# Kernel optimization log

Measured on AMD Instinct MI355X. Metric: run time of the kernel, lower is better.

The kernel has to match this reference:

```python
import jax, jax.numpy as jnp
import numpy as np

B, C, N, L = 64, 32, 500, 12
C_OUT = 32
C_CAT = 9 * C  # (order*(support_len+1)+1)*c_in = 288


def setup_inputs() -> dict:
    key = jax.random.key(0)
    ks = jax.random.split(key, 7)
    x = jax.random.normal(ks[0], (B, C, N, L), dtype=jnp.float32)
    # row-stochastic-ish adjacencies: scale by 1/N to keep hops numerically tame
    A0 = jax.random.uniform(ks[1], (N, N), dtype=jnp.float32) / N
    A1 = jax.random.uniform(ks[2], (N, N), dtype=jnp.float32) / N
    A2 = jax.random.uniform(ks[3], (N, N), dtype=jnp.float32) / N
    A3 = jax.random.uniform(ks[4], (B, N, N), dtype=jnp.float32) / N
    W = jax.random.normal(ks[5], (C_OUT, C_CAT), dtype=jnp.float32) * 0.05
    b = jax.random.normal(ks[6], (C_OUT,), dtype=jnp.float32) * 0.05
    return {"x": x, "A0": A0, "A1": A1, "A2": A2, "A3": A3, "W": W, "b": b}


def reference(x, A0, A1, A2, A3, W, b):
    # x: [B, C, N, L]; A0..A2: [N, N]; A3: [B, N, N]; W: [C_OUT, 9*C]; b: [C_OUT]
    def hop2(h, A):  # static adjacency
        return jnp.einsum('ncvl,vw->ncwl', h, A)

    def hop3(h, A):  # batched (dynamic) adjacency
        return jnp.einsum('ncvl,nvw->ncwl', h, A)

    out = [x]
    for A in (A0, A1, A2):
        x1 = hop2(x, A)
        x2 = hop2(x1, A)
        out.extend([x1, x2])
    x1 = hop3(x, A3)
    x2 = hop3(x1, A3)
    out.extend([x1, x2])

    h = jnp.concatenate(out, axis=1)  # [B, 9C, N, L]
    # 1x1 Conv2d == channel mixing matmul + bias
    h = jnp.einsum('ncvl,oc->novl', h, W) + b[None, :, None, None]
    # dropout in eval mode: identity
    return h
```

## Files before the change

kernel.cpp:

```cpp
#include <hip/hip_runtime.h>

typedef unsigned short u16;
typedef __bf16 bf16x8 __attribute__((ext_vector_type(8)));
typedef float f32x4 __attribute__((ext_vector_type(4)));
typedef const unsigned int __attribute__((address_space(1))) gu32;
typedef unsigned int __attribute__((address_space(3))) lu32;

#define NN 500
#define LLc 12
#define CC 32
#define MM 384
#define KP 512
#define MT 96
#define NT2 128
#define XS_S 40
#define AS_S 40
#define CT2_S 136
#define TS_S 384
#define AT_ELS 256000
#define HM_G 12288000L
#define HM_B 192000L
#define HCL_G 12582912L
#define HCL_B 196608L

__device__ __forceinline__ u16 f2bf(float f) {
    union { float f; unsigned u; } cv; cv.f = f;
    unsigned u = cv.u;
    u += 0x7fffu + ((u >> 16) & 1u);
    return (u16)(u >> 16);
}
__device__ __forceinline__ float bf2f(u16 s) {
    union { unsigned u; float f; } cv; cv.u = ((unsigned)s) << 16;
    return cv.f;
}

__global__ __launch_bounds__(256) void prep_all(
    const float* __restrict__ x,
    const float* __restrict__ A0, const float* __restrict__ A1,
    const float* __restrict__ A2, const float* __restrict__ A3,
    u16* __restrict__ At_s, u16* __restrict__ At_b,
    u16* __restrict__ Xt, u16* __restrict__ Xm,
    const float* __restrict__ W, u16* __restrict__ Wp)
{
    __shared__ u16 Ls[MM * 36];
    const int id = blockIdx.x;
    const int t = threadIdx.x;

    if (id < 17152) {
        int rem = id & 255;
        int z  = id >> 8;
        int n0 = (rem & 15) * 32;
        int k0 = (rem >> 4) * 32;
        const float* Ab; u16* Ob;
        if (z == 0)      { Ab = A0; Ob = At_s; }
        else if (z == 1) { Ab = A1; Ob = At_s + (long)AT_ELS; }
        else if (z == 2) { Ab = A2; Ob = At_s + 2L * AT_ELS; }
        else             { Ab = A3 + (long)(z - 3) * NN * NN; Ob = At_b + (long)(z - 3) * AT_ELS; }
        {
            int vl = t >> 3, u = t & 7;
            float4 v = make_float4(0.f, 0.f, 0.f, 0.f);
            if (k0 + vl < NN && n0 + 4 * u + 4 <= NN)
                v = *(const float4*)(Ab + (long)(k0 + vl) * NN + n0 + 4 * u);
            int nb = 4 * u;
            Ls[(nb + 0) * 36 + vl] = f2bf(v.x);
            Ls[(nb + 1) * 36 + vl] = f2bf(v.y);
            Ls[(nb + 2) * 36 + vl] = f2bf(v.z);
            Ls[(nb + 3) * 36 + vl] = f2bf(v.w);
        }
        __syncthreads();
        {
            int row = t >> 3, u = t & 7;
            if (n0 + row < NN)
                *(uint2*)(Ob + (long)(n0 + row) * KP + k0 + 4 * u) = *(const uint2*)(&Ls[row * 36 + 4 * u]);
        }
    } else if (id < 18176) {
        int jj = id - 17152;
        int v0 = (jj & 15) * 32;
        int b  = jj >> 4;
        #pragma unroll
        for (int j = 0; j < 12; ++j) {
            int f = t + 256 * j;
            int c = f / 96;
            int r = f - c * 96;
            int vl = r / 3;
            int l3 = (r - vl * 3) * 4;
            float4 v = make_float4(0.f, 0.f, 0.f, 0.f);
            if (v0 + vl < NN)
                v = *(const float4*)(x + ((long)b * CC + c) * (NN * LLc) + (long)(v0 + vl) * LLc + l3);
            int mb = (c * LLc + l3) * 36 + vl;
            Ls[mb]       = f2bf(v.x);
            Ls[mb + 36]  = f2bf(v.y);
            Ls[mb + 72]  = f2bf(v.z);
            Ls[mb + 108] = f2bf(v.w);
        }
        __syncthreads();
        #pragma unroll
        for (int j = 0; j < 12; ++j) {
            int f = t + 256 * j;
            int row = f >> 3, u = f & 7;
            *(uint2*)(Xt + ((long)b * MM + row) * KP + v0 + 4 * u) = *(const uint2*)(&Ls[row * 36 + 4 * u]);
        }
        if (Xm) {
            u16* Xb = Xm + (long)b * HM_B;
            #pragma unroll
            for (int j = 0; j < 6; ++j) {
                int f = t + 256 * j;
                int vl = f & 31;
                int lq = f >> 5;
                int l  = lq % 12;
                int cq = lq / 12;
                if (v0 + vl < NN) {
                    union { u16 s[8]; uint4 v; } pk;
                    #pragma unroll
                    for (int c8 = 0; c8 < 8; ++c8)
                        pk.s[c8] = Ls[((cq * 8 + c8) * 12 + l) * 36 + vl];
                    *(uint4*)(Xb + ((long)(l * NN + v0 + vl)) * 32 + cq * 8) = pk.v;
                }
            }
        }
    } else {
        int idx = (id - 18176) * 256 + t;
        int j    = idx & 7;
        int lane = (idx >> 3) & 63;
        int p    = (idx >> 9) & 1;
        int mt   = (idx >> 10) & 1;
        int g    = idx >> 11;
        int o  = mt * 16 + (lane & 15);
        int kk = g * 32 + (lane >> 4) * 8 + j;
        float wv = W[o * 288 + kk];
        u16 hi = f2bf(wv);
        Wp[idx] = (p == 0) ? hi : f2bf(wv - bf2f(hi));
    }
}

__global__ __launch_bounds__(256, 3) void hop_fast8(
    const u16* __restrict__ Xsrc, long x_gstride, long x_bstride,
    const u16* __restrict__ At_s,
    const u16* __restrict__ At_b,
    u16* __restrict__ Hcl,
    u16* __restrict__ HmArg)
{
    __shared__ __align__(16) u16 smem[21504];
    u16* Ct = smem;

    const int t = threadIdx.x;
    const int lane = t & 63;
    const int wv = t >> 6;
    const int f0 = blockIdx.x + 4 * (blockIdx.y + 4 * blockIdx.z);
    const int w  = (f0 & 7) * 2048 + (f0 >> 3);
    const int zc = w >> 4;
    const int rem = w & 15;
    const int bx = rem & 3;
    const int my = rem >> 2;
    const int g  = zc & 3;
    const int b  = zc >> 2;
    const int n0 = bx * NT2;
    const int m0 = my * 96;
    const int cb = my * 8;
    const int ln  = lane & 15;
    const int q16 = lane >> 4;

    const u16* Ab = (g < 3) ? (At_s + (long)g * AT_ELS) : (At_b + (long)b * AT_ELS);
    const u16* Xb = Xsrc + (long)g * x_gstride + (long)b * x_bstride;

    const int rbase = lane >> 2;
    const int coff  = (((lane & 3) ^ ((lane >> 3) & 3)) << 3);
    const int rsel  = ((q16 ^ ((ln >> 1) & 3)) << 3);

    auto STAGE = [&](int kk, int pb) {
        char* base = (char*)smem + pb * 14336;
        if (wv < 2) {
            #pragma unroll
            for (int j = 0; j < 4; ++j) {
                int r16 = wv * 4 + j;
                const u16* src = Ab + (long)(n0 + r16 * 16 + rbase) * KP + kk + coff;
                __builtin_amdgcn_global_load_lds((gu32*)src, (lu32*)(base + r16 * 1024), 16, 0, 0);
            }
        } else {
            #pragma unroll
            for (int j = 0; j < 3; ++j) {
                int r16 = (wv - 2) * 3 + j;
                const u16* src = Xb + (long)(m0 + r16 * 16 + rbase) * KP + kk + coff;
                __builtin_amdgcn_global_load_lds((gu32*)src, (lu32*)(base + 8192 + r16 * 1024), 16, 0, 0);
            }
        }
    };

    f32x4 acc[2][6];
    #pragma unroll
    for (int ns = 0; ns < 2; ++ns)
        #pragma unroll
        for (int i = 0; i < 6; ++i)
            #pragma unroll
            for (int r = 0; r < 4; ++r) acc[ns][i][r] = 0.f;

    auto COMPUTE = [&](int pb) {
        const u16* As = smem + pb * 7168;
        const u16* Xs = As + 4096;
        bf16x8 b0 = *(const bf16x8*)(&As[(wv * 32 + ln) * 32 + rsel]);
        bf16x8 b1 = *(const bf16x8*)(&As[(wv * 32 + 16 + ln) * 32 + rsel]);
        __builtin_amdgcn_s_setprio(1);
        #pragma unroll
        for (int i = 0; i < 6; ++i) {
            bf16x8 af = *(const bf16x8*)(&Xs[(i * 16 + ln) * 32 + rsel]);
            acc[0][i] = __builtin_amdgcn_mfma_f32_16x16x32_bf16(af, b0, acc[0][i], 0, 0, 0);
            acc[1][i] = __builtin_amdgcn_mfma_f32_16x16x32_bf16(af, b1, acc[1][i], 0, 0, 0);
        }
        __builtin_amdgcn_s_setprio(0);
    };

    STAGE(0, 0);
    STAGE(32, 1);
    int c0 = 0, c1 = 1, c2 = 2;
    #pragma unroll 1
    for (int s = 0; s < 15; ++s) {
        if (wv < 2) asm volatile("s_waitcnt vmcnt(4)" ::: "memory");
        else        asm volatile("s_waitcnt vmcnt(3)" ::: "memory");
        __builtin_amdgcn_s_barrier();
        __builtin_amdgcn_sched_barrier(0);
        if (s <= 13) STAGE(32 * (s + 2), c2);
        COMPUTE(c0);
        int tmp = c0; c0 = c1; c1 = c2; c2 = tmp;
    }
    asm volatile("s_waitcnt vmcnt(0)" ::: "memory");
    __builtin_amdgcn_s_barrier();
    __builtin_amdgcn_sched_barrier(0);
    COMPUTE(c0);

    __syncthreads();
    #pragma unroll
    for (int ns = 0; ns < 2; ++ns) {
        int col = wv * 32 + ns * 16 + ln;
        #pragma unroll
        for (int i6 = 0; i6 < 6; ++i6) {
            int rb = i6 * 16 + (lane >> 4) * 4;
            #pragma unroll
            for (int r = 0; r < 4; ++r)
                Ct[(rb + r) * CT2_S + col] = f2bf(acc[ns][i6][r]);
        }
    }
    __syncthreads();
    if (Hcl) {
        u16* Ocl = Hcl + (long)g * HCL_G + (long)b * HCL_B;
        #pragma unroll
        for (int j = 0; j < 12; ++j) {
            int f = t + 256 * j;
            int row = f >> 5, u = f & 31;
            int n = n0 + 4 * u;
            uint2 v = make_uint2(0u, 0u);
            if (n < NN) v = *(const uint2*)(&Ct[row * CT2_S + 4 * u]);
            *(uint2*)(Ocl + (long)(m0 + row) * KP + n) = v;
        }
    }
    {
        u16* Om = HmArg + (long)g * HM_G + (long)b * HM_B;
        #pragma unroll
        for (int j = 0; j < 6; ++j) {
            int f = t + 256 * j;
            int n_l = f & 127;
            int l   = f >> 7;
            int n = n0 + n_l;
            if (n < NN) {
                union { u16 s[8]; uint4 v; } pk;
                #pragma unroll
                for (int c8 = 0; c8 < 8; ++c8)
                    pk.s[c8] = Ct[(c8 * 12 + l) * CT2_S + n_l];
                *(uint4*)(Om + ((long)(l * NN + n)) * 32 + cb) = pk.v;
            }
        }
    }
}

__global__ __launch_bounds__(256, 3) void hop_fast7(
    const u16* __restrict__ Xsrc, long x_gstride, long x_bstride,
    const u16* __restrict__ At_s,
    const u16* __restrict__ At_b,
    u16* __restrict__ Hout, long h_gstride)
{
    __shared__ __align__(16) u16 smem[24576];
    u16* Ct = smem;

    const int t = threadIdx.x;
    const int lane = t & 63;
    const int wv = t >> 6;
    const int f0 = blockIdx.x + 4 * (blockIdx.y + 3 * blockIdx.z);
    const int w  = (f0 & 7) * 384 + (f0 >> 3);
    const int zc = w / 12;
    const int rem = w - zc * 12;
    const int bx = rem & 3;
    const int by = rem >> 2;
    const int g  = zc & 3;
    const int b  = zc >> 2;
    const int n0 = bx * 128;
    const int m0 = by * 128;
    const int ln  = lane & 15;
    const int q16 = lane >> 4;

    const u16* Ab = (g < 3) ? (At_s + (long)g * AT_ELS) : (At_b + (long)b * AT_ELS);
    const u16* Xb = Xsrc + (long)g * x_gstride + (long)b * x_bstride;
    u16* Ob = Hout + (long)g * h_gstride + (long)b * ((long)MM * KP);

    const int rbase = lane >> 2;
    const int coff  = (((lane & 3) ^ ((lane >> 3) & 3)) << 3);
    const int rsel  = ((q16 ^ ((ln >> 1) & 3)) << 3);

    auto STAGE = [&](int kk, int pb) {
        #pragma unroll
        for (int j = 0; j < 4; ++j) {
            int o = (wv * 4 + j) << 10;
            const u16* src;
            if (o < 8192) src = Ab + (long)(n0 + (o >> 6) + rbase) * KP + kk + coff;
            else          src = Xb + (long)(m0 + (o >> 6) - 128 + rbase) * KP + kk + coff;
            __builtin_amdgcn_global_load_lds((gu32*)src,
                (lu32*)((char*)smem + pb * 16384 + o), 16, 0, 0);
        }
    };

    f32x4 acc[2][8];
    #pragma unroll
    for (int ns = 0; ns < 2; ++ns)
        #pragma unroll
        for (int i = 0; i < 8; ++i)
            #pragma unroll
            for (int r = 0; r < 4; ++r) acc[ns][i][r] = 0.f;

    auto COMPUTE = [&](int pb) {
        const u16* As = smem + pb * 8192;
        const u16* Xs = As + 4096;
        bf16x8 b0 = *(const bf16x8*)(&As[(wv * 32 + ln) * 32 + rsel]);
        bf16x8 b1 = *(const bf16x8*)(&As[(wv * 32 + 16 + ln) * 32 + rsel]);
        __builtin_amdgcn_s_setprio(1);
        #pragma unroll
        for (int i = 0; i < 8; ++i) {
            bf16x8 af = *(const bf16x8*)(&Xs[(i * 16 + ln) * 32 + rsel]);
            acc[0][i] = __builtin_amdgcn_mfma_f32_16x16x32_bf16(af, b0, acc[0][i], 0, 0, 0);
            acc[1][i] = __builtin_amdgcn_mfma_f32_16x16x32_bf16(af, b1, acc[1][i], 0, 0, 0);
        }
        __builtin_amdgcn_s_setprio(0);
    };

    STAGE(0, 0);
    STAGE(32, 1);
    int c0 = 0, c1 = 1, c2 = 2;
    #pragma unroll 1
    for (int s = 0; s < 15; ++s) {
        asm volatile("s_waitcnt vmcnt(4)" ::: "memory");
        __builtin_amdgcn_s_barrier();
        __builtin_amdgcn_sched_barrier(0);
        if (s <= 13) STAGE(32 * (s + 2), c2);
        COMPUTE(c0);
        int tmp = c0; c0 = c1; c1 = c2; c2 = tmp;
    }
    asm volatile("s_waitcnt vmcnt(0)" ::: "memory");
    __builtin_amdgcn_s_barrier();
    __builtin_amdgcn_sched_barrier(0);
    COMPUTE(c0);

    #pragma unroll
    for (int h = 0; h < 2; ++h) {
        __syncthreads();
        #pragma unroll
        for (int ns = 0; ns < 2; ++ns) {
            int col = wv * 32 + ns * 16 + ln;
            #pragma unroll
            for (int i4 = 0; i4 < 4; ++i4) {
                int rb = i4 * 16 + (lane >> 4) * 4;
                #pragma unroll
                for (int r = 0; r < 4; ++r)
                    Ct[(rb + r) * CT2_S + col] = f2bf(acc[ns][h * 4 + i4][r]);
            }
        }
        __syncthreads();
        #pragma unroll
        for (int j = 0; j < 8; ++j) {
            int f = t + 256 * j;
            int row = f >> 5, u = f & 31;
            int n = n0 + 4 * u;
            uint2 v = make_uint2(0u, 0u);
            if (n < NN) v = *(const uint2*)(&Ct[row * CT2_S + 4 * u]);
            *(uint2*)(Ob + (long)(m0 + h * 64 + row) * KP + n) = v;
        }
    }
}

__global__ __launch_bounds__(512, 4) void mix_stream(
    const u16* __restrict__ Xm,
    const u16* __restrict__ Hm,
    const u16* __restrict__ Wp,
    const float* __restrict__ bias,
    float* __restrict__ out)
{
    __shared__ __align__(16) float Ct[12496];

    const int t   = threadIdx.x;
    const int wg  = blockIdx.y * 8 + blockIdx.x;
    const int swz = (wg & 7) * 64 + (wg >> 3);
    const int bx  = swz & 7;
    const int b   = swz >> 3;
    const int n0  = bx * 64;
    const int w    = t >> 6;
    const int lane = t & 63;
    const int kq   = lane >> 4;
    const int ln   = lane & 15;

    f32x4 acc[6][2];
    #pragma unroll
    for (int i = 0; i < 6; ++i)
        #pragma unroll
        for (int m = 0; m < 2; ++m)
            #pragma unroll
            for (int r = 0; r < 4; ++r) acc[i][m][r] = 0.f;

    #pragma unroll 1
    for (int g = 0; g < 9; ++g) {
        const u16* src;
        if (g == 0) src = Xm + (long)b * HM_B;
        else {
            int gg = g - 1;
            int buf = (gg & 1) ? 4 + (gg >> 1) : (gg >> 1);
            src = Hm + (long)buf * HM_G + (long)b * HM_B;
        }
        uint4 wf[2][2];
        #pragma unroll
        for (int mt = 0; mt < 2; ++mt)
            #pragma unroll
            for (int p = 0; p < 2; ++p)
                wf[mt][p] = *(const uint4*)(Wp + ((((g * 2 + mt) * 2 + p) * 64 + lane) * 8));
        #pragma unroll
        for (int i = 0; i < 6; ++i) {
            int ct = w * 6 + i;
            int l  = ct >> 2;
            int n  = n0 + ((ct & 3) << 4) + ln;
            uint4 fbv = make_uint4(0u, 0u, 0u, 0u);
            if (n < NN) fbv = *(const uint4*)(src + ((long)(l * NN + n)) * 32 + kq * 8);
            bf16x8 fb = *(const bf16x8*)&fbv;
            acc[i][0] = __builtin_amdgcn_mfma_f32_16x16x32_bf16(*(const bf16x8*)&wf[0][0], fb, acc[i][0], 0, 0, 0);
            acc[i][0] = __builtin_amdgcn_mfma_f32_16x16x32_bf16(*(const bf16x8*)&wf[0][1], fb, acc[i][0], 0, 0, 0);
            acc[i][1] = __builtin_amdgcn_mfma_f32_16x16x32_bf16(*(const bf16x8*)&wf[1][0], fb, acc[i][1], 0, 0, 0);
            acc[i][1] = __builtin_amdgcn_mfma_f32_16x16x32_bf16(*(const bf16x8*)&wf[1][1], fb, acc[i][1], 0, 0, 0);
        }
    }

    #pragma unroll
    for (int mt = 0; mt < 2; ++mt) {
        __syncthreads();
        #pragma unroll
        for (int i = 0; i < 6; ++i) {
            int col = (w * 6 + i) * 16 + ln;
            #pragma unroll
            for (int r = 0; r < 4; ++r)
                Ct[(kq * 4 + r) * 781 + col] = acc[i][mt][r];
        }
        __syncthreads();
        int o16 = t >> 5, u = t & 31;
        int og = mt * 16 + o16;
        float bs = bias[og];
        float* ob = out + (((long)b * CC + og) * NN + n0) * 12L;
        #pragma unroll
        for (int j2 = 0; j2 < 2; ++j2) {
            int n = u + 32 * j2;
            if (n0 + n < NN) {
                float v[12];
                #pragma unroll
                for (int l = 0; l < 12; ++l) v[l] = Ct[o16 * 781 + l * 64 + n] + bs;
                #pragma unroll
                for (int q = 0; q < 3; ++q)
                    *(float4*)(ob + (long)n * 12 + q * 4) = *(const float4*)&v[q * 4];
            }
        }
    }
}

__global__ __launch_bounds__(512, 4) void mix_mfma(
    const u16* __restrict__ Xt,
    const u16* __restrict__ H,
    const u16* __restrict__ Wp,
    const float* __restrict__ bias,
    float* __restrict__ out,
    long h_gs, long h_bs, int h_rs)
{
    __shared__ __align__(16) char smem[50176];
    u16*   Ls = (u16*)smem;
    float* Ct = (float*)smem;

    const int t   = threadIdx.x;
    const int wg  = blockIdx.y * 8 + blockIdx.x;
    const int swz = (wg & 7) * 64 + (wg >> 3);
    const int bx  = swz & 7;
    const int b   = swz >> 3;
    const int n0  = bx * 64;
    const int w    = t >> 6;
    const int lane = t & 63;
    const int kq   = lane >> 4;
    const int ln   = lane & 15;
    const int srow   = lane >> 3;
    const int schunk = (lane & 7) * 8;

    f32x4 acc[6][2];
    #pragma unroll
    for (int i = 0; i < 6; ++i)
        #pragma unroll
        for (int m = 0; m < 2; ++m)
            #pragma unroll
            for (int r = 0; r < 4; ++r) acc[i][m][r] = 0.f;

    #pragma unroll 1
    for (int g = 0; g < 9; ++g) {
        const u16* base; int rs;
        if (g == 0) { base = Xt + (long)b * (MM * KP); rs = KP; }
        else {
            int gg = g - 1;
            int buf = (gg & 1) ? 4 + (gg >> 1) : (gg >> 1);
            base = H + (long)buf * h_gs + (long)b * h_bs; rs = h_rs;
        }
        __syncthreads();
        #pragma unroll
        for (int i = 0; i < 6; ++i) {
            int r0 = (w * 6 + i) * 8;
            const u16* src = base + (long)(r0 + srow) * rs + n0 + schunk;
            __builtin_amdgcn_global_load_lds((gu32*)src, (lu32*)(Ls + r0 * 64), 16, 0, 0);
        }
        asm volatile("s_waitcnt vmcnt(0)" ::: "memory");
        __syncthreads();
        uint4 wf[2][2];
        #pragma unroll
        for (int mt = 0; mt < 2; ++mt)
            #pragma unroll
            for (int p = 0; p < 2; ++p)
                wf[mt][p] = *(const uint4*)(Wp + ((((g * 2 + mt) * 2 + p) * 64 + lane) * 8));
        #pragma unroll
        for (int i = 0; i < 6; ++i) {
            int ct = w * 6 + i;
            int off0 = kq * 6144 + (ct >> 2) * 64 + (ct & 3) * 16 + ln;
            union { u16 s[8]; bf16x8 v; } fb;
            #pragma unroll
            for (int j = 0; j < 8; ++j) fb.s[j] = Ls[off0 + j * 768];
            #pragma unroll
            for (int mt = 0; mt < 2; ++mt) {
                acc[i][mt] = __builtin_amdgcn_mfma_f32_16x16x32_bf16(*(const bf16x8*)&wf[mt][0], fb.v, acc[i][mt], 0, 0, 0);
                acc[i][mt] = __builtin_amdgcn_mfma_f32_16x16x32_bf16(*(const bf16x8*)&wf[mt][1], fb.v, acc[i][mt], 0, 0, 0);
            }
        }
    }

    #pragma unroll
    for (int mt = 0; mt < 2; ++mt) {
        __syncthreads();
        #pragma unroll
        for (int i = 0; i < 6; ++i) {
            int col = (w * 6 + i) * 16 + ln;
            #pragma unroll
            for (int r = 0; r < 4; ++r)
                Ct[(kq * 4 + r) * 781 + col] = acc[i][mt][r];
        }
        __syncthreads();
        int o16 = t >> 5, u = t & 31;
        int og = mt * 16 + o16;
        float bs = bias[og];
        float* ob = out + (((long)b * CC + og) * NN + n0) * 12L;
        #pragma unroll
        for (int j2 = 0; j2 < 2; ++j2) {
            int n = u + 32 * j2;
            if (n0 + n < NN) {
                float v[12];
                #pragma unroll
                for (int l = 0; l < 12; ++l) v[l] = Ct[o16 * 781 + l * 64 + n] + bs;
                #pragma unroll
                for (int q = 0; q < 3; ++q)
                    *(float4*)(ob + (long)n * 12 + q * 4) = *(const float4*)&v[q * 4];
            }
        }
    }
}

__global__ __launch_bounds__(256) void atrans_all(
    const float* __restrict__ A0, const float* __restrict__ A1,
    const float* __restrict__ A2, const float* __restrict__ A3,
    u16* __restrict__ At_s, u16* __restrict__ At_b)
{
    __shared__ u16 Ls[32 * 36];
    const int t = threadIdx.x;
    const int n0 = blockIdx.x * 32;
    const int k0 = blockIdx.y * 32;
    const int z = blockIdx.z;
    const float* Ab; u16* Ob;
    if (z == 0)      { Ab = A0; Ob = At_s; }
    else if (z == 1) { Ab = A1; Ob = At_s + (long)AT_ELS; }
    else if (z == 2) { Ab = A2; Ob = At_s + 2L * AT_ELS; }
    else             { Ab = A3 + (long)(z - 3) * NN * NN; Ob = At_b + (long)(z - 3) * AT_ELS; }
    {
        int vl = t >> 3, u = t & 7;
        float4 v = make_float4(0.f, 0.f, 0.f, 0.f);
        if (k0 + vl < NN && n0 + 4 * u + 4 <= NN)
            v = *(const float4*)(Ab + (long)(k0 + vl) * NN + n0 + 4 * u);
        int nb = 4 * u;
        Ls[(nb + 0) * 36 + vl] = f2bf(v.x);
        Ls[(nb + 1) * 36 + vl] = f2bf(v.y);
        Ls[(nb + 2) * 36 + vl] = f2bf(v.z);
        Ls[(nb + 3) * 36 + vl] = f2bf(v.w);
    }
    __syncthreads();
    {
        int row = t >> 3, u = t & 7;
        if (n0 + row < NN)
            *(uint2*)(Ob + (long)(n0 + row) * KP + k0 + 4 * u) = *(const uint2*)(&Ls[row * 36 + 4 * u]);
    }
}

__global__ __launch_bounds__(256) void xpose_kernel(
    const float* __restrict__ x, u16* __restrict__ Xt)
{
    __shared__ u16 Ls[MM * 36];
    const int t = threadIdx.x;
    const int v0 = blockIdx.x * 32;
    const int b  = blockIdx.y;
    #pragma unroll
    for (int j = 0; j < 12; ++j) {
        int f = t + 256 * j;
        int c = f / 96;
        int r = f - c * 96;
        int vl = r / 3;
        int l3 = (r - vl * 3) * 4;
        float4 v = make_float4(0.f, 0.f, 0.f, 0.f);
        if (v0 + vl < NN)
            v = *(const float4*)(x + ((long)b * CC + c) * (NN * LLc) + (long)(v0 + vl) * LLc + l3);
        int mb = (c * LLc + l3) * 36 + vl;
        Ls[mb]       = f2bf(v.x);
        Ls[mb + 36]  = f2bf(v.y);
        Ls[mb + 72]  = f2bf(v.z);
        Ls[mb + 108] = f2bf(v.w);
    }
    __syncthreads();
    #pragma unroll
    for (int j = 0; j < 12; ++j) {
        int f = t + 256 * j;
        int row = f >> 3, u = f & 7;
        *(uint2*)(Xt + ((long)b * MM + row) * KP + v0 + 4 * u) = *(const uint2*)(&Ls[row * 36 + 4 * u]);
    }
}

__global__ __launch_bounds__(256, 4) void hop_fast(
    const u16* __restrict__ Xsrc, long x_bstride, int x_rstride, int x_klim,
    const u16* __restrict__ At,   long a_bstride,
    u16* __restrict__ hout)
{
    __shared__ __align__(16) u16 smem[13056];
    u16* As = smem;
    u16* Xs = smem + 5120;
    u16* Ct = smem;

    const int t = threadIdx.x;
    const int lane = t & 63;
    const int wv = t >> 6;
    const int n0 = blockIdx.x * NT2;
    const int m0 = blockIdx.y * MT;
    const int b  = blockIdx.z;
    const int ln = lane & 15;
    const int q8 = (lane >> 4) * 8;

    const u16* Ab = At + (long)b * a_bstride;
    const u16* Xb = Xsrc + (long)b * x_bstride;

    uint2 pa[4], px[3];
    auto loadA = [&](int k0) {
        #pragma unroll
        for (int j = 0; j < 4; ++j) {
            int f = t + 256 * j;
            int n = f >> 3, u = f & 7;
            uint2 v = make_uint2(0u, 0u);
            if (n0 + n < NN)
                v = *(const uint2*)(Ab + (long)(n0 + n) * KP + k0 + 4 * u);
            pa[j] = v;
        }
    };
    auto loadX = [&](int k0) {
        #pragma unroll
        for (int j = 0; j < 3; ++j) {
            int f = t + 256 * j;
            int r = f >> 3, u = f & 7;
            int k = k0 + 4 * u;
            uint2 v = make_uint2(0u, 0u);
            if (k < x_klim)
                v = *(const uint2*)(Xb + (long)(m0 + r) * x_rstride + k);
            px[j] = v;
        }
    };

    f32x4 acc[2][6];
    #pragma unroll
    for (int ns = 0; ns < 2; ++ns)
        #pragma unroll
        for (int i = 0; i < 6; ++i)
            #pragma unroll
            for (int r = 0; r < 4; ++r) acc[ns][i][r] = 0.f;

    loadA(0);
    loadX(0);
    #pragma unroll 1
    for (int s = 0; s < 16; ++s) {
        __syncthreads();
        #pragma unroll
        for (int j = 0; j < 4; ++j) {
            int f = t + 256 * j;
            *(uint2*)(&As[(f >> 3) * AS_S + 4 * (f & 7)]) = pa[j];
        }
        #pragma unroll
        for (int j = 0; j < 3; ++j) {
            int f = t + 256 * j;
            *(uint2*)(&Xs[(f >> 3) * XS_S + 4 * (f & 7)]) = px[j];
        }
        if (s < 15) {
            loadA(32 * (s + 1));
            loadX(32 * (s + 1));
        }
        __syncthreads();
        bf16x8 af[6];
        #pragma unroll
        for (int i = 0; i < 6; ++i)
            af[i] = *(const bf16x8*)(&Xs[(i * 16 + ln) * XS_S + q8]);
        #pragma unroll
        for (int ns = 0; ns < 2; ++ns) {
            bf16x8 bfr = *(const bf16x8*)(&As[(wv * 32 + ns * 16 + ln) * AS_S + q8]);
            #pragma unroll
            for (int i = 0; i < 6; ++i)
                acc[ns][i] = __builtin_amdgcn_mfma_f32_16x16x32_bf16(af[i], bfr, acc[ns][i], 0, 0, 0);
        }
    }

    __syncthreads();
    #pragma unroll
    for (int ns = 0; ns < 2; ++ns) {
        int col = wv * 32 + ns * 16 + ln;
        #pragma unroll
        for (int i = 0; i < 6; ++i) {
            int rb = i * 16 + (lane >> 4) * 4;
            #pragma unroll
            for (int r = 0; r < 4; ++r)
                Ct[(rb + r) * CT2_S + col] = f2bf(acc[ns][i][r]);
        }
    }
    __syncthreads();
    u16* Ob = hout + (long)b * ((long)MM * NN);
    #pragma unroll
    for (int j = 0; j < 12; ++j) {
        int f = t + 256 * j;
        int row = f >> 5, u = f & 31;
        int n = n0 + 4 * u;
        if (n < NN)
            *(uint2*)(Ob + (long)(m0 + row) * NN + n) = *(const uint2*)(&Ct[row * CT2_S + 4 * u]);
    }
}

__global__ __launch_bounds__(256, 2) void mix_kernel(
    const float* __restrict__ x,
    const u16* __restrict__ h1,
    const u16* __restrict__ h2,
    const float* __restrict__ W,
    const float* __restrict__ bias,
    int blk1, int blk2,
    float* __restrict__ out, int init)
{
    __shared__ __align__(16) float smem[CC * TS_S + 3 * 1056];
    float* ts = smem;
    float* Ws = smem + CC * TS_S;

    const int t = threadIdx.x;
    const int b = blockIdx.y;
    const int w0 = blockIdx.x * 32;
    const int o  = t & 15;
    const int wg = (t >> 4) & 7;
    const int lh = t >> 7;

    #pragma unroll
    for (int j = 0; j < 4; ++j) {
        int f = t + 256 * j;
        int oo = f & 31, c = f >> 5;
        Ws[c * 33 + oo]        = W[oo * 288 + blk1 * 32 + c];
        Ws[1056 + c * 33 + oo] = W[oo * 288 + blk2 * 32 + c];
        if (init) Ws[2112 + c * 33 + oo] = W[oo * 288 + c];
    }

    float acc2[2][4][6];
    #pragma unroll
    for (int a = 0; a < 2; ++a)
        #pragma unroll
        for (int q = 0; q < 4; ++q)
            #pragma unroll
            for (int l = 0; l < 6; ++l) acc2[a][q][l] = 0.f;

    auto stage_h = [&](const u16* h) {
        #pragma unroll
        for (int j = 0; j < 12; ++j) {
            int f = t + 256 * j;
            int row = f >> 3, u = f & 7;
            int w = w0 + 4 * u;
            uint2 raw = make_uint2(0u, 0u);
            if (w < NN)
                raw = *(const uint2*)(h + ((long)b * MM + row) * NN + w);
            int c = row / 12;
            int l = row - c * 12;
            float* dst = &ts[c * TS_S + l * 32 + 4 * u];
            dst[0] = bf2f((u16)(raw.x & 0xffffu));
            dst[1] = bf2f((u16)(raw.x >> 16));
            dst[2] = bf2f((u16)(raw.y & 0xffffu));
            dst[3] = bf2f((u16)(raw.y >> 16));
        }
    };
    auto accum = [&](const float* Wg) {
        for (int c = 0; c < CC; ++c) {
            float w1 = Wg[c * 33 + o];
            float w2 = Wg[c * 33 + o + 16];
            #pragma unroll
            for (int l6 = 0; l6 < 6; ++l6) {
                const float4 hv = *(const float4*)(&ts[c * TS_S + (lh * 6 + l6) * 32 + wg * 4]);
                acc2[0][0][l6] += w1 * hv.x;
                acc2[0][1][l6] += w1 * hv.y;
                acc2[0][2][l6] += w1 * hv.z;
                acc2[0][3][l6] += w1 * hv.w;
                acc2[1][0][l6] += w2 * hv.x;
                acc2[1][1][l6] += w2 * hv.y;
                acc2[1][2][l6] += w2 * hv.z;
                acc2[1][3][l6] += w2 * hv.w;
            }
        }
    };

    if (init) {
        #pragma unroll
        for (int j = 0; j < 12; ++j) {
            int f = t + 256 * j;
            int c = f / 96;
            int r = f - c * 96;
            int w = r / 3;
            int q = r - w * 3;
            float4 v = make_float4(0.f, 0.f, 0.f, 0.f);
            if (w0 + w < NN)
                v = *(const float4*)(x + ((long)b * CC + c) * (NN * LLc) + (long)(w0 + w) * LLc + q * 4);
            float* dst = &ts[c * TS_S + (q * 4) * 32 + w];
            dst[0]  = v.x; dst[32] = v.y; dst[64] = v.z; dst[96] = v.w;
        }
        __syncthreads();
        accum(Ws + 2112);
        __syncthreads();
    }
    stage_h(h1);
    __syncthreads();
    accum(Ws);
    __syncthreads();
    stage_h(h2);
    __syncthreads();
    accum(Ws + 1056);

    #pragma unroll
    for (int oh = 0; oh < 2; ++oh) {
        int oo = o + 16 * oh;
        float bs = init ? bias[oo] : 0.f;
        #pragma unroll
        for (int q = 0; q < 4; ++q) {
            int w = w0 + wg * 4 + q;
            if (w < NN) {
                float* op = out + ((long)b * CC + oo) * (NN * LLc) + (long)w * LLc + lh * 6;
                #pragma unroll
                for (int p = 0; p < 3; ++p) {
                    float2* pp = (float2*)op + p;
                    float2 v;
                    if (init) {
                        v.x = bs + acc2[oh][q][2 * p];
                        v.y = bs + acc2[oh][q][2 * p + 1];
                    } else {
                        v = *pp;
                        v.x += acc2[oh][q][2 * p];
                        v.y += acc2[oh][q][2 * p + 1];
                    }
                    *pp = v;
                }
            }
        }
    }
}

extern "C" void kernel_launch(void* const* d_in, const int* in_sizes, int n_in,
                              void* d_out, int out_size, void* d_ws, size_t ws_size,
                              hipStream_t stream) {
    const float* x    = (const float*)d_in[0];
    const float* A0   = (const float*)d_in[1];
    const float* A1   = (const float*)d_in[2];
    const float* A2   = (const float*)d_in[3];
    const float* A3   = (const float*)d_in[4];
    const float* W    = (const float*)d_in[5];
    const float* bias = (const float*)d_in[6];
    float* out = (float*)d_out;
    char* ws = (char*)d_ws;

    const size_t AT_BYTES  = (size_t)AT_ELS * 2;
    const size_t A3T_BYTES = 64 * AT_BYTES;
    const size_t XT_BYTES  = (size_t)64 * MM * KP * 2;
    const size_t WPK_BYTES = 36864;
    const size_t HB2_ELS   = (size_t)64 * MM * KP;
    const size_t H8B_PAD   = 8 * HB2_ELS * 2;
    const size_t need4 = H8B_PAD + 3 * AT_BYTES + A3T_BYTES + XT_BYTES + WPK_BYTES;

    const size_t HCL_BYTES = 4 * HB2_ELS * 2;
    const size_t HM_BYTES  = 8 * (size_t)HM_G * 2;
    const size_t XM_BYTES  = 64 * (size_t)HM_B * 2;
    const size_t need5 = HCL_BYTES + HM_BYTES + 3 * AT_BYTES + A3T_BYTES
                       + XT_BYTES + XM_BYTES + WPK_BYTES;

    dim3 blk(256);

    if (ws_size >= need5) {
        u16* Hcl  = (u16*)ws;
        u16* Hm   = (u16*)(ws + HCL_BYTES);
        u16* At_s = (u16*)(ws + HCL_BYTES + HM_BYTES);
        u16* A3t  = At_s + 3L * AT_ELS;
        u16* Xt   = (u16*)((char*)A3t + A3T_BYTES);
        u16* Xm   = Xt + (size_t)64 * MM * KP;
        u16* Wpk  = Xm + 64 * (size_t)HM_B;

        prep_all<<<dim3(18248), blk, 0, stream>>>(x, A0, A1, A2, A3, At_s, A3t, Xt, Xm, W, Wpk);
        hop_fast8<<<dim3(4, 4, 1024), blk, 0, stream>>>(
            Xt, 0L, (long)MM * KP, At_s, A3t, Hcl, Hm);
        hop_fast8<<<dim3(4, 4, 1024), blk, 0, stream>>>(
            Hcl, (long)HCL_G, (long)HCL_B, At_s, A3t, (u16*)nullptr, Hm + 4 * HM_G);
        mix_stream<<<dim3(8, 64), dim3(512), 0, stream>>>(Xm, Hm, Wpk, bias, out);
        return;
    }

    if (ws_size >= need4) {
        u16* Hb   = (u16*)ws;
        u16* At_s = (u16*)(ws + H8B_PAD);
        u16* A3t  = At_s + 3L * AT_ELS;
        u16* Xt   = (u16*)(ws + H8B_PAD + 3 * AT_BYTES + A3T_BYTES);
        u16* Wpk  = Xt + (size_t)64 * MM * KP;

        prep_all<<<dim3(18248), blk, 0, stream>>>(x, A0, A1, A2, A3, At_s, A3t, Xt, (u16*)nullptr, W, Wpk);
        hop_fast7<<<dim3(4, 3, 256), blk, 0, stream>>>(
            Xt, 0L, (long)MM * KP, At_s, A3t, Hb, (long)HB2_ELS);
        hop_fast7<<<dim3(4, 3, 256), blk, 0, stream>>>(
            Hb, (long)HB2_ELS, (long)MM * KP, At_s, A3t,
            Hb + 4 * HB2_ELS, (long)HB2_ELS);
        mix_mfma<<<dim3(8, 64), dim3(512), 0, stream>>>(
            Xt, Hb, Wpk, bias, out, (long)HB2_ELS, (long)MM * KP, KP);
        return;
    }

    const size_t HBUF_ELS  = (size_t)64 * MM * NN;
    const size_t H_BYTES   = HBUF_ELS * 2;
    const size_t need_at   = 2 * H_BYTES + 3 * AT_BYTES + A3T_BYTES;

    u16* H1 = (u16*)ws;
    u16* H2 = (u16*)(ws + H_BYTES);
    u16* At0 = (u16*)(ws + 2 * H_BYTES);
    u16* A3t = At0 + 3L * AT_ELS;
    u16* Xt  = (u16*)(ws + need_at);

    dim3 fgrid(4, 4, 64);
    dim3 mgrid(16, 64);

    xpose_kernel<<<dim3(16, 64), blk, 0, stream>>>(x, Xt);
    atrans_all<<<dim3(16, 16, 67), blk, 0, stream>>>(A0, A1, A2, A3, At0, A3t);

    const long XT_BS = (long)MM * KP;
    const long H_BS  = (long)MM * NN;
    u16* Atp[4] = {At0, At0 + (long)AT_ELS, At0 + 2L * AT_ELS, A3t};

    for (int i = 0; i < 4; ++i) {
        long a_bs = (i == 3) ? (long)AT_ELS : 0;
        hop_fast<<<fgrid, blk, 0, stream>>>(Xt, XT_BS, KP, KP, Atp[i], a_bs, H1);
        hop_fast<<<fgrid, blk, 0, stream>>>(H1, H_BS, NN, NN, Atp[i], a_bs, H2);
        mix_kernel<<<mgrid, blk, 0, stream>>>(i == 0 ? x : nullptr, H1, H2, W, bias,
                                              2 * i + 1, 2 * i + 2, out, i == 0 ? 1 : 0);
    }
}
```

Measured before the change: 365.7 us.

## Use hybrid layouts: channel-major first hop, mix-friendly second hop with 192-row tiles

Removes the dual-layout hop_fast8 path and the Xm pre-transpose. The first hop (hop_fast7) now writes only the channel-major layout. A new hop_fast10 computes the second hop with 192-row M tiles and writes only the mix-friendly [l, n, c] layout with padded N=512. The mixing kernel reads x and the first-hop outputs through LDS staging, and reads the second-hop outputs directly in the mix layout. This avoids writing each hop output in two layouts and drops the Xm buffer, at the cost of a simpler two-stage pipeline in the second hop and a hybrid read path in the mix kernel.

```diff
diff --git a/kernel.cpp b/kernel.cpp
--- a/kernel.cpp
+++ b/kernel.cpp
@@ -18,10 +18,8 @@
 #define CT2_S 136
 #define TS_S 384
 #define AT_ELS 256000
-#define HM_G 12288000L
-#define HM_B 192000L
-#define HCL_G 12582912L
-#define HCL_B 196608L
+#define HB2_ELS 12582912L
+#define HB2_B   196608L
 
 __device__ __forceinline__ u16 f2bf(float f) {
     union { float f; unsigned u; } cv; cv.f = f;
@@ -39,7 +37,7 @@
     const float* __restrict__ A0, const float* __restrict__ A1,
     const float* __restrict__ A2, const float* __restrict__ A3,
     u16* __restrict__ At_s, u16* __restrict__ At_b,
-    u16* __restrict__ Xt, u16* __restrict__ Xm,
+    u16* __restrict__ Xt,
     const float* __restrict__ W, u16* __restrict__ Wp)
 {
     __shared__ u16 Ls[MM * 36];
@@ -100,24 +98,6 @@
             int row = f >> 3, u = f & 7;
             *(uint2*)(Xt + ((long)b * MM + row) * KP + v0 + 4 * u) = *(const uint2*)(&Ls[row * 36 + 4 * u]);
         }
-        if (Xm) {
-            u16* Xb = Xm + (long)b * HM_B;
-            #pragma unroll
-            for (int j = 0; j < 6; ++j) {
-                int f = t + 256 * j;
-                int vl = f & 31;
-                int lq = f >> 5;
-                int l  = lq % 12;
-                int cq = lq / 12;
-                if (v0 + vl < NN) {
-                    union { u16 s[8]; uint4 v; } pk;
-                    #pragma unroll
-                    for (int c8 = 0; c8 < 8; ++c8)
-                        pk.s[c8] = Ls[((cq * 8 + c8) * 12 + l) * 36 + vl];
-                    *(uint4*)(Xb + ((long)(l * NN + v0 + vl)) * 32 + cq * 8) = pk.v;
-                }
-            }
-        }
     } else {
         int idx = (id - 18176) * 256 + t;
         int j    = idx & 7;
@@ -130,144 +110,6 @@
         float wv = W[o * 288 + kk];
         u16 hi = f2bf(wv);
         Wp[idx] = (p == 0) ? hi : f2bf(wv - bf2f(hi));
-    }
-}
-
-__global__ __launch_bounds__(256, 3) void hop_fast8(
-    const u16* __restrict__ Xsrc, long x_gstride, long x_bstride,
-    const u16* __restrict__ At_s,
-    const u16* __restrict__ At_b,
-    u16* __restrict__ Hcl,
-    u16* __restrict__ HmArg)
-{
-    __shared__ __align__(16) u16 smem[21504];
-    u16* Ct = smem;
-
-    const int t = threadIdx.x;
-    const int lane = t & 63;
-    const int wv = t >> 6;
-    const int f0 = blockIdx.x + 4 * (blockIdx.y + 4 * blockIdx.z);
-    const int w  = (f0 & 7) * 2048 + (f0 >> 3);
-    const int zc = w >> 4;
-    const int rem = w & 15;
-    const int bx = rem & 3;
-    const int my = rem >> 2;
-    const int g  = zc & 3;
-    const int b  = zc >> 2;
-    const int n0 = bx * NT2;
-    const int m0 = my * 96;
-    const int cb = my * 8;
-    const int ln  = lane & 15;
-    const int q16 = lane >> 4;
-
-    const u16* Ab = (g < 3) ? (At_s + (long)g * AT_ELS) : (At_b + (long)b * AT_ELS);
-    const u16* Xb = Xsrc + (long)g * x_gstride + (long)b * x_bstride;
-
-    const int rbase = lane >> 2;
-    const int coff  = (((lane & 3) ^ ((lane >> 3) & 3)) << 3);
-    const int rsel  = ((q16 ^ ((ln >> 1) & 3)) << 3);
-
-    auto STAGE = [&](int kk, int pb) {
-        char* base = (char*)smem + pb * 14336;
-        if (wv < 2) {
-            #pragma unroll
-            for (int j = 0; j < 4; ++j) {
-                int r16 = wv * 4 + j;
-                const u16* src = Ab + (long)(n0 + r16 * 16 + rbase) * KP + kk + coff;
-                __builtin_amdgcn_global_load_lds((gu32*)src, (lu32*)(base + r16 * 1024), 16, 0, 0);
-            }
-        } else {
-            #pragma unroll
-            for (int j = 0; j < 3; ++j) {
-                int r16 = (wv - 2) * 3 + j;
-                const u16* src = Xb + (long)(m0 + r16 * 16 + rbase) * KP + kk + coff;
-                __builtin_amdgcn_global_load_lds((gu32*)src, (lu32*)(base + 8192 + r16 * 1024), 16, 0, 0);
-            }
-        }
-    };
-
-    f32x4 acc[2][6];
-    #pragma unroll
-    for (int ns = 0; ns < 2; ++ns)
-        #pragma unroll
-        for (int i = 0; i < 6; ++i)
-            #pragma unroll
-            for (int r = 0; r < 4; ++r) acc[ns][i][r] = 0.f;
-
-    auto COMPUTE = [&](int pb) {
-        const u16* As = smem + pb * 7168;
-        const u16* Xs = As + 4096;
-        bf16x8 b0 = *(const bf16x8*)(&As[(wv * 32 + ln) * 32 + rsel]);
-        bf16x8 b1 = *(const bf16x8*)(&As[(wv * 32 + 16 + ln) * 32 + rsel]);
-        __builtin_amdgcn_s_setprio(1);
-        #pragma unroll
-        for (int i = 0; i < 6; ++i) {
-            bf16x8 af = *(const bf16x8*)(&Xs[(i * 16 + ln) * 32 + rsel]);
-            acc[0][i] = __builtin_amdgcn_mfma_f32_16x16x32_bf16(af, b0, acc[0][i], 0, 0, 0);
-            acc[1][i] = __builtin_amdgcn_mfma_f32_16x16x32_bf16(af, b1, acc[1][i], 0, 0, 0);
-        }
-        __builtin_amdgcn_s_setprio(0);
-    };
-
-    STAGE(0, 0);
-    STAGE(32, 1);
-    int c0 = 0, c1 = 1, c2 = 2;
-    #pragma unroll 1
-    for (int s = 0; s < 15; ++s) {
-        if (wv < 2) asm volatile("s_waitcnt vmcnt(4)" ::: "memory");
-        else        asm volatile("s_waitcnt vmcnt(3)" ::: "memory");
-        __builtin_amdgcn_s_barrier();
-        __builtin_amdgcn_sched_barrier(0);
-        if (s <= 13) STAGE(32 * (s + 2), c2);
-        COMPUTE(c0);
-        int tmp = c0; c0 = c1; c1 = c2; c2 = tmp;
-    }
-    asm volatile("s_waitcnt vmcnt(0)" ::: "memory");
-    __builtin_amdgcn_s_barrier();
-    __builtin_amdgcn_sched_barrier(0);
-    COMPUTE(c0);
-
-    __syncthreads();
-    #pragma unroll
-    for (int ns = 0; ns < 2; ++ns) {
-        int col = wv * 32 + ns * 16 + ln;
-        #pragma unroll
-        for (int i6 = 0; i6 < 6; ++i6) {
-            int rb = i6 * 16 + (lane >> 4) * 4;
-            #pragma unroll
-            for (int r = 0; r < 4; ++r)
-                Ct[(rb + r) * CT2_S + col] = f2bf(acc[ns][i6][r]);
-        }
-    }
-    __syncthreads();
-    if (Hcl) {
-        u16* Ocl = Hcl + (long)g * HCL_G + (long)b * HCL_B;
-        #pragma unroll
-        for (int j = 0; j < 12; ++j) {
-            int f = t + 256 * j;
-            int row = f >> 5, u = f & 31;
-            int n = n0 + 4 * u;
-            uint2 v = make_uint2(0u, 0u);
-            if (n < NN) v = *(const uint2*)(&Ct[row * CT2_S + 4 * u]);
-            *(uint2*)(Ocl + (long)(m0 + row) * KP + n) = v;
-        }
-    }
-    {
-        u16* Om = HmArg + (long)g * HM_G + (long)b * HM_B;
-        #pragma unroll
-        for (int j = 0; j < 6; ++j) {
-            int f = t + 256 * j;
-            int n_l = f & 127;
-            int l   = f >> 7;
-            int n = n0 + n_l;
-            if (n < NN) {
-                union { u16 s[8]; uint4 v; } pk;
-                #pragma unroll
-                for (int c8 = 0; c8 < 8; ++c8)
-                    pk.s[c8] = Ct[(c8 * 12 + l) * CT2_S + n_l];
-                *(uint4*)(Om + ((long)(l * NN + n)) * 32 + cb) = pk.v;
-            }
-        }
     }
 }
 
@@ -383,101 +225,121 @@
     }
 }
 
-__global__ __launch_bounds__(512, 4) void mix_stream(
-    const u16* __restrict__ Xm,
-    const u16* __restrict__ Hm,
+__global__ __launch_bounds__(256, 3) void hop_fast10(
+    const u16* __restrict__ Xsrc, long x_gstride, long x_bstride,
+    const u16* __restrict__ At_s,
+    const u16* __restrict__ At_b,
+    u16* __restrict__ Hm)
+{
+    __shared__ __align__(16) u16 smem[20480];
+    u16* Ct = smem;
+
+    const int t = threadIdx.x;
+    const int lane = t & 63;
+    const int wv = t >> 6;
+    const int f0 = blockIdx.x + 4 * blockIdx.y + 8 * blockIdx.z;
+    const int w  = (f0 & 7) * 256 + (f0 >> 3);
+    const int bx = w & 3;
+    const int by = (w >> 2) & 1;
+    const int zc = w >> 3;
+    const int g  = zc & 3;
+    const int b  = zc >> 2;
+    const int n0 = bx * NT2;
+    const int m0 = by * 192;
+    const int ln  = lane & 15;
+    const int q16 = lane >> 4;
+
+    const u16* Ab = (g < 3) ? (At_s + (long)g * AT_ELS) : (At_b + (long)b * AT_ELS);
+    const u16* Xb = Xsrc + (long)g * x_gstride + (long)b * x_bstride;
+    u16* Om = Hm + (long)g * HB2_ELS + (long)b * HB2_B;
+
+    const int rbase = lane >> 2;
+    const int coff  = (((lane & 3) ^ ((lane >> 3) & 3)) << 3);
+    const int rsel  = ((q16 ^ ((ln >> 1) & 3)) << 3);
+
+    auto STAGE = [&](int kk, int pb) {
+        #pragma unroll
+        for (int j = 0; j < 5; ++j) {
+            int o = (wv * 5 + j) << 10;
+            const u16* src;
+            if (o < 8192) src = Ab + (long)(n0 + (o >> 6) + rbase) * KP + kk + coff;
+            else          src = Xb + (long)(m0 + (o >> 6) - 128 + rbase) * KP + kk + coff;
+            __builtin_amdgcn_global_load_lds((gu32*)src,
+                (lu32*)((char*)smem + pb * 20480 + o), 16, 0, 0);
+        }
+    };
+
+    f32x4 acc[2][12];
+    #pragma unroll
+    for (int ns = 0; ns < 2; ++ns)
+        #pragma unroll
+        for (int i = 0; i < 12; ++i)
+            #pragma unroll
+            for (int r = 0; r < 4; ++r) acc[ns][i][r] = 0.f;
+
+    STAGE(0, 0);
+    asm volatile("s_waitcnt vmcnt(0)" ::: "memory");
+    __syncthreads();
+
+    #pragma unroll 1
+    for (int s = 0; s < 16; ++s) {
+        const int pb = s & 1;
+        if (s < 15) STAGE(32 * (s + 1), pb ^ 1);
+        const u16* As = smem + pb * 10240;
+        const u16* Xs = As + 4096;
+        const int rowA0 = wv * 32 + ln;
+        bf16x8 b0 = *(const bf16x8*)(&As[rowA0 * 32 + rsel]);
+        bf16x8 b1 = *(const bf16x8*)(&As[(rowA0 + 16) * 32 + rsel]);
+        #pragma unroll
+        for (int i = 0; i < 12; ++i) {
+            bf16x8 af = *(const bf16x8*)(&Xs[(i * 16 + ln) * 32 + rsel]);
+            acc[0][i] = __builtin_amdgcn_mfma_f32_16x16x32_bf16(af, b0, acc[0][i], 0, 0, 0);
+            acc[1][i] = __builtin_amdgcn_mfma_f32_16x16x32_bf16(af, b1, acc[1][i], 0, 0, 0);
+        }
+        asm volatile("s_waitcnt vmcnt(0)" ::: "memory");
+        __syncthreads();
+    }
+
+    #pragma unroll
+    for (int h = 0; h < 2; ++h) {
+        __syncthreads();
+        #pragma unroll
+        for (int ns = 0; ns < 2; ++ns) {
+            int col = wv * 32 + ns * 16 + ln;
+            #pragma unroll
+            for (int i6 = 0; i6 < 6; ++i6) {
+                int rb = i6 * 16 + (lane >> 4) * 4;
+                #pragma unroll
+                for (int r = 0; r < 4; ++r)
+                    Ct[(rb + r) * CT2_S + col] = f2bf(acc[ns][h * 6 + i6][r]);
+            }
+        }
+        __syncthreads();
+        int cb = by * 16 + h * 8;
+        #pragma unroll
+        for (int j = 0; j < 6; ++j) {
+            int f = t + 256 * j;
+            int n_l = f & 127;
+            int l   = f >> 7;
+            int n = n0 + n_l;
+            if (n < NN) {
+                union { u16 s[8]; uint4 v; } pk;
+                #pragma unroll
+                for (int c8 = 0; c8 < 8; ++c8)
+                    pk.s[c8] = Ct[(c8 * 12 + l) * CT2_S + n_l];
+                *(uint4*)(Om + ((long)(l * 512 + n)) * 32 + cb) = pk.v;
+            }
+        }
+    }
+}
+
+__global__ __launch_bounds__(512, 4) void mix_hyb(
+    const u16* __restrict__ Xt,
+    const u16* __restrict__ Hcl,
+    const u16* __restrict__ H2m,
     const u16* __restrict__ Wp,
     const float* __restrict__ bias,
     float* __restrict__ out)
-{
-    __shared__ __align__(16) float Ct[12496];
-
-    const int t   = threadIdx.x;
-    const int wg  = blockIdx.y * 8 + blockIdx.x;
-    const int swz = (wg & 7) * 64 + (wg >> 3);
-    const int bx  = swz & 7;
-    const int b   = swz >> 3;
-    const int n0  = bx * 64;
-    const int w    = t >> 6;
-    const int lane = t & 63;
-    const int kq   = lane >> 4;
-    const int ln   = lane & 15;
-
-    f32x4 acc[6][2];
-    #pragma unroll
-    for (int i = 0; i < 6; ++i)
-        #pragma unroll
-        for (int m = 0; m < 2; ++m)
-            #pragma unroll
-            for (int r = 0; r < 4; ++r) acc[i][m][r] = 0.f;
-
-    #pragma unroll 1
-    for (int g = 0; g < 9; ++g) {
-        const u16* src;
-        if (g == 0) src = Xm + (long)b * HM_B;
-        else {
-            int gg = g - 1;
-            int buf = (gg & 1) ? 4 + (gg >> 1) : (gg >> 1);
-            src = Hm + (long)buf * HM_G + (long)b * HM_B;
-        }
-        uint4 wf[2][2];
-        #pragma unroll
-        for (int mt = 0; mt < 2; ++mt)
-            #pragma unroll
-            for (int p = 0; p < 2; ++p)
-                wf[mt][p] = *(const uint4*)(Wp + ((((g * 2 + mt) * 2 + p) * 64 + lane) * 8));
-        #pragma unroll
-        for (int i = 0; i < 6; ++i) {
-            int ct = w * 6 + i;
-            int l  = ct >> 2;
-            int n  = n0 + ((ct & 3) << 4) + ln;
-            uint4 fbv = make_uint4(0u, 0u, 0u, 0u);
-            if (n < NN) fbv = *(const uint4*)(src + ((long)(l * NN + n)) * 32 + kq * 8);
-            bf16x8 fb = *(const bf16x8*)&fbv;
-            acc[i][0] = __builtin_amdgcn_mfma_f32_16x16x32_bf16(*(const bf16x8*)&wf[0][0], fb, acc[i][0], 0, 0, 0);
-            acc[i][0] = __builtin_amdgcn_mfma_f32_16x16x32_bf16(*(const bf16x8*)&wf[0][1], fb, acc[i][0], 0, 0, 0);
-            acc[i][1] = __builtin_amdgcn_mfma_f32_16x16x32_bf16(*(const bf16x8*)&wf[1][0], fb, acc[i][1], 0, 0, 0);
-            acc[i][1] = __builtin_amdgcn_mfma_f32_16x16x32_bf16(*(const bf16x8*)&wf[1][1], fb, acc[i][1], 0, 0, 0);
-        }
-    }
-
-    #pragma unroll
-    for (int mt = 0; mt < 2; ++mt) {
-        __syncthreads();
-        #pragma unroll
-        for (int i = 0; i < 6; ++i) {
-            int col = (w * 6 + i) * 16 + ln;
-            #pragma unroll
-            for (int r = 0; r < 4; ++r)
-                Ct[(kq * 4 + r) * 781 + col] = acc[i][mt][r];
-        }
-        __syncthreads();
-        int o16 = t >> 5, u = t & 31;
-        int og = mt * 16 + o16;
-        float bs = bias[og];
-        float* ob = out + (((long)b * CC + og) * NN + n0) * 12L;
-        #pragma unroll
-        for (int j2 = 0; j2 < 2; ++j2) {
-            int n = u + 32 * j2;
-            if (n0 + n < NN) {
-                float v[12];
-                #pragma unroll
-                for (int l = 0; l < 12; ++l) v[l] = Ct[o16 * 781 + l * 64 + n] + bs;
-                #pragma unroll
-                for (int q = 0; q < 3; ++q)
-                    *(float4*)(ob + (long)n * 12 + q * 4) = *(const float4*)&v[q * 4];
-            }
-        }
-    }
-}
-
-__global__ __launch_bounds__(512, 4) void mix_mfma(
-    const u16* __restrict__ Xt,
-    const u16* __restrict__ H,
-    const u16* __restrict__ Wp,
-    const float* __restrict__ bias,
-    float* __restrict__ out,
-    long h_gs, long h_bs, int h_rs)
 {
     __shared__ __align__(16) char smem[50176];
     u16*   Ls = (u16*)smem;
@@ -506,39 +368,51 @@
 
     #pragma unroll 1
     for (int g = 0; g < 9; ++g) {
-        const u16* base; int rs;
-        if (g == 0) { base = Xt + (long)b * (MM * KP); rs = KP; }
-        else {
-            int gg = g - 1;
-            int buf = (gg & 1) ? 4 + (gg >> 1) : (gg >> 1);
-            base = H + (long)buf * h_gs + (long)b * h_bs; rs = h_rs;
-        }
-        __syncthreads();
-        #pragma unroll
-        for (int i = 0; i < 6; ++i) {
-            int r0 = (w * 6 + i) * 8;
-            const u16* src = base + (long)(r0 + srow) * rs + n0 + schunk;
-            __builtin_amdgcn_global_load_lds((gu32*)src, (lu32*)(Ls + r0 * 64), 16, 0, 0);
-        }
-        asm volatile("s_waitcnt vmcnt(0)" ::: "memory");
-        __syncthreads();
         uint4 wf[2][2];
         #pragma unroll
         for (int mt = 0; mt < 2; ++mt)
             #pragma unroll
             for (int p = 0; p < 2; ++p)
                 wf[mt][p] = *(const uint4*)(Wp + ((((g * 2 + mt) * 2 + p) * 64 + lane) * 8));
-        #pragma unroll
-        for (int i = 0; i < 6; ++i) {
-            int ct = w * 6 + i;
-            int off0 = kq * 6144 + (ct >> 2) * 64 + (ct & 3) * 16 + ln;
-            union { u16 s[8]; bf16x8 v; } fb;
-            #pragma unroll
-            for (int j = 0; j < 8; ++j) fb.s[j] = Ls[off0 + j * 768];
-            #pragma unroll
-            for (int mt = 0; mt < 2; ++mt) {
-                acc[i][mt] = __builtin_amdgcn_mfma_f32_16x16x32_bf16(*(const bf16x8*)&wf[mt][0], fb.v, acc[i][mt], 0, 0, 0);
-                acc[i][mt] = __builtin_amdgcn_mfma_f32_16x16x32_bf16(*(const bf16x8*)&wf[mt][1], fb.v, acc[i][mt], 0, 0, 0);
+
+        if (g == 0 || (g & 1)) {
+            const u16* base = (g == 0) ? (Xt + (long)b * (MM * KP))
+                                       : (Hcl + (long)((g - 1) >> 1) * HB2_ELS + (long)b * HB2_B);
+            __syncthreads();
+            #pragma unroll
+            for (int i = 0; i < 6; ++i) {
+                int r0 = (w * 6 + i) * 8;
+                const u16* src = base + (long)(r0 + srow) * KP + n0 + schunk;
+                __builtin_amdgcn_global_load_lds((gu32*)src, (lu32*)(Ls + r0 * 64), 16, 0, 0);
+            }
+            asm volatile("s_waitcnt vmcnt(0)" ::: "memory");
+            __syncthreads();
+            #pragma unroll
+            for (int i = 0; i < 6; ++i) {
+                int ct = w * 6 + i;
+                int off0 = kq * 6144 + (ct >> 2) * 64 + (ct & 3) * 16 + ln;
+                union { u16 s[8]; bf16x8 v; } fb;
+                #pragma unroll
+                for (int j = 0; j < 8; ++j) fb.s[j] = Ls[off0 + j * 768];
+                acc[i][0] = __builtin_amdgcn_mfma_f32_16x16x32_bf16(*(const bf16x8*)&wf[0][0], fb.v, acc[i][0], 0, 0, 0);
+                acc[i][0] = __builtin_amdgcn_mfma_f32_16x16x32_bf16(*(const bf16x8*)&wf[0][1], fb.v, acc[i][0], 0, 0, 0);
+                acc[i][1] = __builtin_amdgcn_mfma_f32_16x16x32_bf16(*(const bf16x8*)&wf[1][0], fb.v, acc[i][1], 0, 0, 0);
+                acc[i][1] = __builtin_amdgcn_mfma_f32_16x16x32_bf16(*(const bf16x8*)&wf[1][1], fb.v, acc[i][1], 0, 0, 0);
+            }
+        } else {
+            const u16* src = H2m + (long)((g - 2) >> 1) * HB2_ELS + (long)b * HB2_B;
+            #pragma unroll
+            for (int i = 0; i < 6; ++i) {
+                int ct = w * 6 + i;
+                int l  = ct >> 2;
+                int n  = n0 + ((ct & 3) << 4) + ln;
+                uint4 fbv = make_uint4(0u, 0u, 0u, 0u);
+                if (n < NN) fbv = *(const uint4*)(src + ((long)(l * 512 + n)) * 32 + kq * 8);
+                bf16x8 fb = *(const bf16x8*)&fbv;
+                acc[i][0] = __builtin_amdgcn_mfma_f32_16x16x32_bf16(*(const bf16x8*)&wf[0][0], fb, acc[i][0], 0, 0, 0);
+                acc[i][0] = __builtin_amdgcn_mfma_f32_16x16x32_bf16(*(const bf16x8*)&wf[0][1], fb, acc[i][0], 0, 0, 0);
+                acc[i][1] = __builtin_amdgcn_mfma_f32_16x16x32_bf16(*(const bf16x8*)&wf[1][0], fb, acc[i][1], 0, 0, 0);
+                acc[i][1] = __builtin_amdgcn_mfma_f32_16x16x32_bf16(*(const bf16x8*)&wf[1][1], fb, acc[i][1], 0, 0, 0);
             }
         }
     }
@@ -896,51 +770,27 @@
     const size_t A3T_BYTES = 64 * AT_BYTES;
     const size_t XT_BYTES  = (size_t)64 * MM * KP * 2;
     const size_t WPK_BYTES = 36864;
-    const size_t HB2_ELS   = (size_t)64 * MM * KP;
-    const size_t H8B_PAD   = 8 * HB2_ELS * 2;
-    const size_t need4 = H8B_PAD + 3 * AT_BYTES + A3T_BYTES + XT_BYTES + WPK_BYTES;
-
-    const size_t HCL_BYTES = 4 * HB2_ELS * 2;
-    const size_t HM_BYTES  = 8 * (size_t)HM_G * 2;
-    const size_t XM_BYTES  = 64 * (size_t)HM_B * 2;
-    const size_t need5 = HCL_BYTES + HM_BYTES + 3 * AT_BYTES + A3T_BYTES
-                       + XT_BYTES + XM_BYTES + WPK_BYTES;
+    const size_t HCL_BYTES = 4 * (size_t)HB2_ELS * 2;
+    const size_t H2M_BYTES = 4 * (size_t)HB2_ELS * 2;
+    const size_t need4 = HCL_BYTES + H2M_BYTES + 3 * AT_BYTES + A3T_BYTES
+                       + XT_BYTES + WPK_BYTES;
 
     dim3 blk(256);
 
-    if (ws_size >= need5) {
+    if (ws_size >= need4) {
         u16* Hcl  = (u16*)ws;
-        u16* Hm   = (u16*)(ws + HCL_BYTES);
-        u16* At_s = (u16*)(ws + HCL_BYTES + HM_BYTES);
+        u16* H2m  = (u16*)(ws + HCL_BYTES);
+        u16* At_s = (u16*)(ws + HCL_BYTES + H2M_BYTES);
         u16* A3t  = At_s + 3L * AT_ELS;
         u16* Xt   = (u16*)((char*)A3t + A3T_BYTES);
-        u16* Xm   = Xt + (size_t)64 * MM * KP;
-        u16* Wpk  = Xm + 64 * (size_t)HM_B;
-
-        prep_all<<<dim3(18248), blk, 0, stream>>>(x, A0, A1, A2, A3, At_s, A3t, Xt, Xm, W, Wpk);
-        hop_fast8<<<dim3(4, 4, 1024), blk, 0, stream>>>(
-            Xt, 0L, (long)MM * KP, At_s, A3t, Hcl, Hm);
-        hop_fast8<<<dim3(4, 4, 1024), blk, 0, stream>>>(
-            Hcl, (long)HCL_G, (long)HCL_B, At_s, A3t, (u16*)nullptr, Hm + 4 * HM_G);
-        mix_stream<<<dim3(8, 64), dim3(512), 0, stream>>>(Xm, Hm, Wpk, bias, out);
-        return;
-    }
-
-    if (ws_size >= need4) {
-        u16* Hb   = (u16*)ws;
-        u16* At_s = (u16*)(ws + H8B_PAD);
-        u16* A3t  = At_s + 3L * AT_ELS;
-        u16* Xt   = (u16*)(ws + H8B_PAD + 3 * AT_BYTES + A3T_BYTES);
         u16* Wpk  = Xt + (size_t)64 * MM * KP;
 
-        prep_all<<<dim3(18248), blk, 0, stream>>>(x, A0, A1, A2, A3, At_s, A3t, Xt, (u16*)nullptr, W, Wpk);
+        prep_all<<<dim3(18248), blk, 0, stream>>>(x, A0, A1, A2, A3, At_s, A3t, Xt, W, Wpk);
         hop_fast7<<<dim3(4, 3, 256), blk, 0, stream>>>(
-            Xt, 0L, (long)MM * KP, At_s, A3t, Hb, (long)HB2_ELS);
-        hop_fast7<<<dim3(4, 3, 256), blk, 0, stream>>>(
-            Hb, (long)HB2_ELS, (long)MM * KP, At_s, A3t,
-            Hb + 4 * HB2_ELS, (long)HB2_ELS);
-        mix_mfma<<<dim3(8, 64), dim3(512), 0, stream>>>(
-            Xt, Hb, Wpk, bias, out, (long)HB2_ELS, (long)MM * KP, KP);
+            Xt, 0L, (long)MM * KP, At_s, A3t, Hcl, (long)HB2_ELS);
+        hop_fast10<<<dim3(4, 2, 256), blk, 0, stream>>>(
+            Hcl, (long)HB2_ELS, (long)HB2_B, At_s, A3t, H2m);
+        mix_hyb<<<dim3(8, 64), dim3(512), 0, stream>>>(Xt, Hcl, H2m, Wpk, bias, out);
         return;
     }
 
```

Result: slower. 432.0 us (+18.1%).
